# Kernel optimization log

Hardware: AMD Instinct MI355X
Metric: run time of the kernel (lower is better)

Reference implementation:

```python
import jax, jax.numpy as jnp
import numpy as np

N_EMBD = 1024
N_HEAD = 16
HEAD_DIM = N_EMBD // N_HEAD  # 64
LATENT_DIM = N_EMBD // 2     # 512
B, T = 4, 2048


def setup_inputs() -> dict:
    key = jax.random.key(0)
    ks = jax.random.split(key, 5)
    # weights stored [in, out] so forward is x @ W (equivalent to torch Linear with W.T)
    def init(k, fan_in, fan_out):
        bound = 1.0 / np.sqrt(fan_in)
        return jax.random.uniform(k, (fan_in, fan_out), jnp.float32, -bound, bound)
    return {
        "x": jax.random.normal(ks[0], (B, T, N_EMBD), jnp.float32),
        "Wc_down": init(ks[1], N_EMBD, LATENT_DIM),
        "Wq_up": init(ks[2], LATENT_DIM, N_EMBD),
        "Wkv_up": init(ks[3], LATENT_DIM, 2 * HEAD_DIM),
        "Wc_proj": init(ks[4], N_EMBD, N_EMBD),
    }


def reference(x, Wc_down, Wq_up, Wkv_up, Wc_proj):
    Bsz, Tlen, C = x.shape
    latent = x @ Wc_down                                    # [B,T,latent]
    q = (latent @ Wq_up).reshape(Bsz, Tlen, N_HEAD, HEAD_DIM)  # [B,T,H,D]
    kv = latent @ Wkv_up                                    # [B,T,2D]
    k, v = kv[..., :HEAD_DIM], kv[..., HEAD_DIM:]           # shared across heads (MQA)
    scale = 1.0 / np.sqrt(HEAD_DIM)
    att = jnp.einsum("bthd,bsd->bhts", q, k) * scale        # [B,H,T,T]
    causal = jnp.tril(jnp.ones((Tlen, Tlen), dtype=bool))
    att = jnp.where(causal[None, None], att, -jnp.inf)
    att = jax.nn.softmax(att, axis=-1)
    y = jnp.einsum("bhts,bsd->bthd", att, v).reshape(Bsz, Tlen, C)
    return y @ Wc_proj
```

## Files before the change

kernel.cpp:

```cpp
#include <hip/hip_runtime.h>
#include <hip/hip_bf16.h>


typedef __attribute__((ext_vector_type(8))) short bf16x8;
typedef __attribute__((ext_vector_type(4))) float floatx4;

#define B_   4
#define T_   2048
#define C_   1024
#define H_   16
#define D_   64
#define L_   512
#define QKV_N 1152

__device__ __forceinline__ float EXP2F(float x) {
    float r;
    asm("v_exp_f32 %0, %1" : "=v"(r) : "v"(x));
    return r;
}

__device__ __forceinline__ unsigned short f2bf(float f) {
    unsigned int x = __float_as_uint(f);
    unsigned int r = (x + 0x7fffu + ((x >> 16) & 1u)) >> 16;
    return (unsigned short)r;
}

__device__ __forceinline__ unsigned int cvtpk_bf(float lo, float hi) {
    unsigned int r;
    asm("v_cvt_pk_bf16_f32 %0, %1, %2" : "=v"(r) : "v"(lo), "v"(hi));
    return r;
}

__device__ __forceinline__ void gload_lds16(const unsigned short* g, char* l) {
    __builtin_amdgcn_global_load_lds(
        (const __attribute__((address_space(1))) void*)g,
        (__attribute__((address_space(3))) void*)l,
        16, 0, 0);
}

__global__ void cvt_bf16(const float* __restrict__ X, unsigned short* __restrict__ Xb, int n4) {
    int i = blockIdx.x * 256 + threadIdx.x;
    if (i >= n4) return;
    float4 v = *(const float4*)(X + (size_t)i * 4);
    ushort4 o;
    o.x = f2bf(v.x); o.y = f2bf(v.y); o.z = f2bf(v.z); o.w = f2bf(v.w);
    *(ushort4*)(Xb + (size_t)i * 4) = o;
}

__global__ void wtrans(const float* __restrict__ W, unsigned short* __restrict__ Wt,
                       int K, int N, float scale) {
    int idx = blockIdx.x * 256 + threadIdx.x;
    if (idx >= K * N) return;
    int n = idx / K, k = idx - n * K;
    Wt[idx] = f2bf(W[(size_t)k * N + n] * scale);
}

__global__ void vtrans(const unsigned short* __restrict__ qkv, unsigned short* __restrict__ Vt) {
    int idx = blockIdx.x * 256 + threadIdx.x;
    int t = idx & (T_ - 1);
    int d = (idx >> 11) & 63;
    int b = idx >> 17;
    Vt[idx] = qkv[((size_t)(b * T_ + t)) * QKV_N + 1024 + 64 + d];
}

#define BM 128
#define BN 128
#define BK 64

template <bool F32OUT>
__global__ __launch_bounds__(256) void gemm_bt(const unsigned short* __restrict__ A,
                                               const unsigned short* __restrict__ Bt,
                                               void* __restrict__ Cout,
                                               int M, int N, int K) {
    __shared__ __align__(16) char ldsA[BM * BK * 2];
    __shared__ __align__(16) char ldsB[BN * BK * 2];
    const int tid = threadIdx.x;
    const int lane = tid & 63, wave = tid >> 6;
    const int lrow = lane & 15, lhi = lane >> 4;
    const int bm = blockIdx.y * BM, bn = blockIdx.x * BN;
    const int wm = (wave >> 1) * 64, wn = (wave & 1) * 64;

    floatx4 acc[4][4] = {};

    for (int k0 = 0; k0 < K; k0 += BK) {
#pragma unroll
        for (int i = 0; i < 4; ++i) {
            int c = tid + i * 256;
            int row = c >> 3;
            int sc = ((c & 7) ^ (row & 7)) * 8;
            gload_lds16(A + (size_t)(bm + row) * K + k0 + sc,
                        ldsA + (i * 256 + wave * 64) * 16);
            gload_lds16(Bt + (size_t)(bn + row) * K + k0 + sc,
                        ldsB + (i * 256 + wave * 64) * 16);
        }
        __syncthreads();
#pragma unroll
        for (int kk = 0; kk < 2; ++kk) {
            bf16x8 af[4], bfr[4];
#pragma unroll
            for (int m = 0; m < 4; ++m) {
                int row = wm + m * 16 + lrow;
                int colb = kk * 64 + lhi * 16;
                af[m] = *(const bf16x8*)(ldsA + row * 128 + (colb ^ ((row & 7) << 4)));
            }
#pragma unroll
            for (int n = 0; n < 4; ++n) {
                int row = wn + n * 16 + lrow;
                int colb = kk * 64 + lhi * 16;
                bfr[n] = *(const bf16x8*)(ldsB + row * 128 + (colb ^ ((row & 7) << 4)));
            }
#pragma unroll
            for (int m = 0; m < 4; ++m)
#pragma unroll
                for (int n = 0; n < 4; ++n)
                    acc[m][n] = __builtin_amdgcn_mfma_f32_16x16x32_bf16(af[m], bfr[n], acc[m][n], 0, 0, 0);
        }
        __syncthreads();
    }
#pragma unroll
    for (int m = 0; m < 4; ++m)
#pragma unroll
        for (int n = 0; n < 4; ++n)
#pragma unroll
            for (int r = 0; r < 4; ++r) {
                int row = bm + wm + m * 16 + lhi * 4 + r;
                int col = bn + wn + n * 16 + lrow;
                float v = acc[m][n][r];
                if (F32OUT)
                    ((float*)Cout)[(size_t)row * N + col] = v;
                else
                    ((unsigned short*)Cout)[(size_t)row * N + col] = f2bf(v);
            }
}

__global__ __launch_bounds__(256, 2) void flash(const unsigned short* __restrict__ QKV,
                                                const unsigned short* __restrict__ Vt,
                                                unsigned short* __restrict__ Y) {
    const int id = blockIdx.x;
    const int qt = 7 - (id >> 6);
    const int h = (id >> 2) & 15;
    const int b = id & 3;
    const int tid = threadIdx.x;
    const int lane = tid & 63, wave = tid >> 6;
    const int lrow = lane & 15, lhi = lane >> 4;

    __shared__ __align__(16) char ldsK[3][64 * 128];
    __shared__ __align__(16) char ldsV[3][64 * 128];
    __shared__ __align__(16) char ldsP[4][64 * 128];

    const int qbase = qt * 256 + wave * 64;
    const unsigned short* KV = QKV + 1024;
    const int nst = qt * 4 + 4;

    const unsigned short* kp[2];
    const unsigned short* vp[2];
#pragma unroll
    for (int i = 0; i < 2; ++i) {
        int c = tid + i * 256;
        int row = c >> 3;
        int sc = ((c & 7) ^ (row & 7)) * 8;
        kp[i] = KV + ((size_t)(b * T_ + row)) * QKV_N + sc;
        vp[i] = Vt + ((size_t)(b * 64 + row)) * T_ + sc;
    }

    bf16x8 qf[4][2];
#pragma unroll
    for (int nf = 0; nf < 4; ++nf)
#pragma unroll
        for (int kk = 0; kk < 2; ++kk) {
            int trow = b * T_ + qbase + nf * 16 + lrow;
            int col = h * 64 + kk * 32 + lhi * 8;
            qf[nf][kk] = *(const bf16x8*)(QKV + (size_t)trow * QKV_N + col);
        }

    floatx4 o[4][4] = {};
    floatx4 ol[4] = {};

    const short one_bf = (short)0x3F80;
    const bf16x8 ones8 = {one_bf, one_bf, one_bf, one_bf, one_bf, one_bf, one_bf, one_bf};

    char* kcur = ldsK[0];  char* kstg = ldsK[1];  char* kfre = ldsK[2];
    char* vcur = ldsV[0];  char* vstg = ldsV[1];  char* vfre = ldsV[2];
#pragma unroll
    for (int i = 0; i < 2; ++i) {
        gload_lds16(kp[i], kcur + (i * 256 + wave * 64) * 16);
        gload_lds16(vp[i], vcur + (i * 256 + wave * 64) * 16);
        kp[i] += 64 * QKV_N;
        vp[i] += 64;
    }

    for (int st = 0; st < nst; ++st) {
        const bool more = (st + 1 < nst);
        const long kadj = more ? 0 : -(long)(64 * QKV_N);
        const long vadj = more ? 0 : -64L;
#pragma unroll
        for (int i = 0; i < 2; ++i) {
            gload_lds16(kp[i] + kadj, kstg + (i * 256 + wave * 64) * 16);
            gload_lds16(vp[i] + vadj, vstg + (i * 256 + wave * 64) * 16);
        }
        if (more) {
            kp[0] += 64 * QKV_N; kp[1] += 64 * QKV_N;
            vp[0] += 64;         vp[1] += 64;
        }
        asm volatile("s_waitcnt vmcnt(4)" ::: "memory");
        __builtin_amdgcn_s_barrier();
        __builtin_amdgcn_sched_barrier(0);

        if (st * 64 <= qbase + 63) {
            floatx4 s[4][4] = {};
#pragma unroll
            for (int kk = 0; kk < 2; ++kk) {
                bf16x8 kf[4];
#pragma unroll
                for (int mf = 0; mf < 4; ++mf) {
                    int row = mf * 16 + lrow;
                    int colb = kk * 64 + lhi * 16;
                    kf[mf] = *(const bf16x8*)(kcur + row * 128 + (colb ^ ((row & 7) << 4)));
                }
                __builtin_amdgcn_s_setprio(1);
#pragma unroll
                for (int mf = 0; mf < 4; ++mf)
#pragma unroll
                    for (int nf = 0; nf < 4; ++nf)
                        s[mf][nf] = __builtin_amdgcn_mfma_f32_16x16x32_bf16(kf[mf], qf[nf][kk], s[mf][nf], 0, 0, 0);
                __builtin_amdgcn_s_setprio(0);
            }

#pragma unroll
            for (int nf = 0; nf < 4; ++nf) {
                if (st * 64 + 63 > qbase + nf * 16) {
                    int qg = qbase + nf * 16 + lrow;
#pragma unroll
                    for (int mf = 0; mf < 4; ++mf)
#pragma unroll
                        for (int r = 0; r < 4; ++r) {
                            int sg = st * 64 + mf * 16 + lhi * 4 + r;
                            if (sg > qg) s[mf][nf][r] = -1e30f;
                        }
                }
#pragma unroll
                for (int mf = 0; mf < 4; ++mf)
#pragma unroll
                    for (int rr = 0; rr < 4; ++rr)
                        s[mf][nf][rr] = EXP2F(s[mf][nf][rr]);
            }

#pragma unroll
            for (int mf = 0; mf < 4; ++mf)
#pragma unroll
                for (int nf = 0; nf < 4; ++nf) {
                    uint2 pk;
                    pk.x = cvtpk_bf(s[mf][nf][0], s[mf][nf][1]);
                    pk.y = cvtpk_bf(s[mf][nf][2], s[mf][nf][3]);
                    int row = nf * 16 + lrow;
                    int colb = (mf * 16 + lhi * 4) * 2;
                    *(uint2*)(ldsP[wave] + row * 128 + (colb ^ ((row & 7) << 4))) = pk;
                }

#pragma unroll
            for (int ss = 0; ss < 2; ++ss) {
                bf16x8 pf[4], vf[4];
#pragma unroll
                for (int m = 0; m < 4; ++m) {
                    int row = m * 16 + lrow;
                    int colb = ss * 64 + lhi * 16;
                    pf[m] = *(const bf16x8*)(ldsP[wave] + row * 128 + (colb ^ ((row & 7) << 4)));
                }
#pragma unroll
                for (int dn = 0; dn < 4; ++dn) {
                    int row = dn * 16 + lrow;
                    int colb = ss * 64 + lhi * 16;
                    vf[dn] = *(const bf16x8*)(vcur + row * 128 + (colb ^ ((row & 7) << 4)));
                }
                __builtin_amdgcn_s_setprio(1);
#pragma unroll
                for (int m = 0; m < 4; ++m) {
#pragma unroll
                    for (int dn = 0; dn < 4; ++dn)
                        o[m][dn] = __builtin_amdgcn_mfma_f32_16x16x32_bf16(pf[m], vf[dn], o[m][dn], 0, 0, 0);
                    ol[m] = __builtin_amdgcn_mfma_f32_16x16x32_bf16(pf[m], ones8, ol[m], 0, 0, 0);
                }
                __builtin_amdgcn_s_setprio(0);
            }
        }

        char* t;
        t = kcur; kcur = kstg; kstg = kfre; kfre = t;
        t = vcur; vcur = vstg; vstg = vfre; vfre = t;
    }

#pragma unroll
    for (int m = 0; m < 4; ++m) {
        float linv[4];
#pragma unroll
        for (int rr = 0; rr < 4; ++rr) linv[rr] = __builtin_amdgcn_rcpf(ol[m][rr]);
#pragma unroll
        for (int dn = 0; dn < 4; ++dn)
#pragma unroll
            for (int rr = 0; rr < 4; ++rr) {
                int trow = b * T_ + qbase + m * 16 + lhi * 4 + rr;
                int col = h * 64 + dn * 16 + lrow;
                Y[(size_t)trow * C_ + col] = f2bf(o[m][dn][rr] * linv[rr]);
            }
    }
}

extern "C" void kernel_launch(void* const* d_in, const int* in_sizes, int n_in,
                              void* d_out, int out_size, void* d_ws, size_t ws_size,
                              hipStream_t stream) {
    (void)in_sizes; (void)n_in; (void)out_size; (void)ws_size;
    const float* x   = (const float*)d_in[0];
    const float* Wd  = (const float*)d_in[1];
    const float* Wq  = (const float*)d_in[2];
    const float* Wkv = (const float*)d_in[3];
    const float* Wp  = (const float*)d_in[4];
    float* out = (float*)d_out;
    char* ws = (char*)d_ws;

    const int BT = B_ * T_;
    const float KSC = 0.125f * 1.44269504f;

    unsigned short* xb     = (unsigned short*)(ws + 0);
    unsigned short* wdT    = (unsigned short*)(ws + 16777216);
    unsigned short* wqkvT  = (unsigned short*)(ws + 17825792);
    unsigned short* wpT    = (unsigned short*)(ws + 19005440);
    unsigned short* latent = (unsigned short*)(ws + 21102592);
    unsigned short* qkv    = (unsigned short*)(ws + 29491200);
    unsigned short* vt     = (unsigned short*)(ws + 48365568);
    unsigned short* yb     = xb;

    cvt_bf16<<<(BT * C_ / 4 + 255) / 256, 256, 0, stream>>>(x, xb, BT * C_ / 4);
    wtrans<<<(C_ * L_ + 255) / 256, 256, 0, stream>>>(Wd, wdT, C_, L_, 1.0f);
    wtrans<<<(L_ * C_ + 255) / 256, 256, 0, stream>>>(Wq, wqkvT, L_, C_, KSC);
    wtrans<<<(L_ * 128 + 255) / 256, 256, 0, stream>>>(Wkv, wqkvT + 1024 * 512, L_, 128, 1.0f);
    wtrans<<<(C_ * C_ + 255) / 256, 256, 0, stream>>>(Wp, wpT, C_, C_, 1.0f);

    gemm_bt<false><<<dim3(L_ / BN, BT / BM), 256, 0, stream>>>(xb, wdT, latent, BT, L_, C_);
    gemm_bt<false><<<dim3(QKV_N / BN, BT / BM), 256, 0, stream>>>(latent, wqkvT, qkv, BT, QKV_N, L_);

    vtrans<<<(B_ * 64 * T_ + 255) / 256, 256, 0, stream>>>(qkv, vt);

    flash<<<512, 256, 0, stream>>>(qkv, vt, yb);

    gemm_bt<true><<<dim3(C_ / BN, BT / BM), 256, 0, stream>>>(yb, wpT, out, BT, C_, C_);
}
```

Measured before the change: 156.5 us.

## Double-buffer GEMM LDS, shrink flash query tiles, pass P via permlane swaps

The GEMM now double-buffers its A/B LDS tiles and prefetches the next K slice while computing the current one, so load latency overlaps with MFMA work. The flash kernel halves the query tile per block (128 rows, 32 per wave) and doubles the grid to 1024 blocks with occupancy 3, aiming for better load balance across the causal triangle. The P matrix is rearranged in registers with permlane32/16 swaps instead of a round trip through LDS, which removes the ldsP buffer and its writes and reads. In exchange, smaller query tiles mean each K/V tile is loaded more times, and the GEMM uses twice the LDS.

```diff
diff --git a/kernel.cpp b/kernel.cpp
--- a/kernel.cpp
+++ b/kernel.cpp
@@ -4,6 +4,7 @@
 
 typedef __attribute__((ext_vector_type(8))) short bf16x8;
 typedef __attribute__((ext_vector_type(4))) float floatx4;
+typedef __attribute__((ext_vector_type(4))) unsigned int uintx4;
 
 #define B_   4
 #define T_   2048
@@ -31,6 +32,13 @@
     return r;
 }
 
+__device__ __forceinline__ void pl32(unsigned int& d, unsigned int& s) {
+    asm("v_permlane32_swap_b32 %0, %1" : "+v"(d), "+v"(s));
+}
+__device__ __forceinline__ void pl16(unsigned int& d, unsigned int& s) {
+    asm("v_permlane16_swap_b32 %0, %1" : "+v"(d), "+v"(s));
+}
+
 __device__ __forceinline__ void gload_lds16(const unsigned short* g, char* l) {
     __builtin_amdgcn_global_load_lds(
         (const __attribute__((address_space(1))) void*)g,
@@ -72,28 +80,50 @@
                                                const unsigned short* __restrict__ Bt,
                                                void* __restrict__ Cout,
                                                int M, int N, int K) {
-    __shared__ __align__(16) char ldsA[BM * BK * 2];
-    __shared__ __align__(16) char ldsB[BN * BK * 2];
+    __shared__ __align__(16) char ldsA[2][BM * BK * 2];
+    __shared__ __align__(16) char ldsB[2][BN * BK * 2];
     const int tid = threadIdx.x;
     const int lane = tid & 63, wave = tid >> 6;
     const int lrow = lane & 15, lhi = lane >> 4;
     const int bm = blockIdx.y * BM, bn = blockIdx.x * BN;
     const int wm = (wave >> 1) * 64, wn = (wave & 1) * 64;
 
+    const unsigned short* ap[4];
+    const unsigned short* bp[4];
+#pragma unroll
+    for (int i = 0; i < 4; ++i) {
+        int c = tid + i * 256;
+        int row = c >> 3;
+        int sc = ((c & 7) ^ (row & 7)) * 8;
+        ap[i] = A + (size_t)(bm + row) * K + sc;
+        bp[i] = Bt + (size_t)(bn + row) * K + sc;
+    }
+    const int nk = K >> 6;
     floatx4 acc[4][4] = {};
 
-    for (int k0 = 0; k0 < K; k0 += BK) {
-#pragma unroll
-        for (int i = 0; i < 4; ++i) {
-            int c = tid + i * 256;
-            int row = c >> 3;
-            int sc = ((c & 7) ^ (row & 7)) * 8;
-            gload_lds16(A + (size_t)(bm + row) * K + k0 + sc,
-                        ldsA + (i * 256 + wave * 64) * 16);
-            gload_lds16(Bt + (size_t)(bn + row) * K + k0 + sc,
-                        ldsB + (i * 256 + wave * 64) * 16);
-        }
-        __syncthreads();
+#pragma unroll
+    for (int i = 0; i < 4; ++i) {
+        gload_lds16(ap[i], ldsA[0] + (i * 256 + wave * 64) * 16);
+        gload_lds16(bp[i], ldsB[0] + (i * 256 + wave * 64) * 16);
+        ap[i] += BK; bp[i] += BK;
+    }
+
+    for (int t = 0; t < nk; ++t) {
+        const int cur = t & 1;
+        if (t + 1 < nk) {
+#pragma unroll
+            for (int i = 0; i < 4; ++i) {
+                gload_lds16(ap[i], ldsA[cur ^ 1] + (i * 256 + wave * 64) * 16);
+                gload_lds16(bp[i], ldsB[cur ^ 1] + (i * 256 + wave * 64) * 16);
+                ap[i] += BK; bp[i] += BK;
+            }
+            asm volatile("s_waitcnt vmcnt(8)" ::: "memory");
+        } else {
+            asm volatile("s_waitcnt vmcnt(0)" ::: "memory");
+        }
+        __builtin_amdgcn_s_barrier();
+        __builtin_amdgcn_sched_barrier(0);
+
 #pragma unroll
         for (int kk = 0; kk < 2; ++kk) {
             bf16x8 af[4], bfr[4];
@@ -101,13 +131,13 @@
             for (int m = 0; m < 4; ++m) {
                 int row = wm + m * 16 + lrow;
                 int colb = kk * 64 + lhi * 16;
-                af[m] = *(const bf16x8*)(ldsA + row * 128 + (colb ^ ((row & 7) << 4)));
+                af[m] = *(const bf16x8*)(ldsA[cur] + row * 128 + (colb ^ ((row & 7) << 4)));
             }
 #pragma unroll
             for (int n = 0; n < 4; ++n) {
                 int row = wn + n * 16 + lrow;
                 int colb = kk * 64 + lhi * 16;
-                bfr[n] = *(const bf16x8*)(ldsB + row * 128 + (colb ^ ((row & 7) << 4)));
+                bfr[n] = *(const bf16x8*)(ldsB[cur] + row * 128 + (colb ^ ((row & 7) << 4)));
             }
 #pragma unroll
             for (int m = 0; m < 4; ++m)
@@ -115,7 +145,8 @@
                 for (int n = 0; n < 4; ++n)
                     acc[m][n] = __builtin_amdgcn_mfma_f32_16x16x32_bf16(af[m], bfr[n], acc[m][n], 0, 0, 0);
         }
-        __syncthreads();
+        __builtin_amdgcn_sched_barrier(0);
+        __builtin_amdgcn_s_barrier();
     }
 #pragma unroll
     for (int m = 0; m < 4; ++m)
@@ -133,11 +164,11 @@
             }
 }
 
-__global__ __launch_bounds__(256, 2) void flash(const unsigned short* __restrict__ QKV,
+__global__ __launch_bounds__(256, 3) void flash(const unsigned short* __restrict__ QKV,
                                                 const unsigned short* __restrict__ Vt,
                                                 unsigned short* __restrict__ Y) {
     const int id = blockIdx.x;
-    const int qt = 7 - (id >> 6);
+    const int qt = 15 - (id >> 6);
     const int h = (id >> 2) & 15;
     const int b = id & 3;
     const int tid = threadIdx.x;
@@ -146,11 +177,10 @@
 
     __shared__ __align__(16) char ldsK[3][64 * 128];
     __shared__ __align__(16) char ldsV[3][64 * 128];
-    __shared__ __align__(16) char ldsP[4][64 * 128];
-
-    const int qbase = qt * 256 + wave * 64;
+
+    const int qbase = qt * 128 + wave * 32;
     const unsigned short* KV = QKV + 1024;
-    const int nst = qt * 4 + 4;
+    const int nst = qt * 2 + 2;
 
     const unsigned short* kp[2];
     const unsigned short* vp[2];
@@ -163,9 +193,9 @@
         vp[i] = Vt + ((size_t)(b * 64 + row)) * T_ + sc;
     }
 
-    bf16x8 qf[4][2];
-#pragma unroll
-    for (int nf = 0; nf < 4; ++nf)
+    bf16x8 qf[2][2];
+#pragma unroll
+    for (int nf = 0; nf < 2; ++nf)
 #pragma unroll
         for (int kk = 0; kk < 2; ++kk) {
             int trow = b * T_ + qbase + nf * 16 + lrow;
@@ -173,8 +203,8 @@
             qf[nf][kk] = *(const bf16x8*)(QKV + (size_t)trow * QKV_N + col);
         }
 
-    floatx4 o[4][4] = {};
-    floatx4 ol[4] = {};
+    floatx4 o[2][4] = {};
+    floatx4 ol[2] = {};
 
     const short one_bf = (short)0x3F80;
     const bf16x8 ones8 = {one_bf, one_bf, one_bf, one_bf, one_bf, one_bf, one_bf, one_bf};
@@ -206,8 +236,8 @@
         __builtin_amdgcn_s_barrier();
         __builtin_amdgcn_sched_barrier(0);
 
-        if (st * 64 <= qbase + 63) {
-            floatx4 s[4][4] = {};
+        if (st * 64 <= qbase + 31) {
+            floatx4 s[4][2] = {};
 #pragma unroll
             for (int kk = 0; kk < 2; ++kk) {
                 bf16x8 kf[4];
@@ -221,13 +251,13 @@
 #pragma unroll
                 for (int mf = 0; mf < 4; ++mf)
 #pragma unroll
-                    for (int nf = 0; nf < 4; ++nf)
+                    for (int nf = 0; nf < 2; ++nf)
                         s[mf][nf] = __builtin_amdgcn_mfma_f32_16x16x32_bf16(kf[mf], qf[nf][kk], s[mf][nf], 0, 0, 0);
                 __builtin_amdgcn_s_setprio(0);
             }
 
 #pragma unroll
-            for (int nf = 0; nf < 4; ++nf) {
+            for (int nf = 0; nf < 2; ++nf) {
                 if (st * 64 + 63 > qbase + nf * 16) {
                     int qg = qbase + nf * 16 + lrow;
 #pragma unroll
@@ -245,27 +275,24 @@
                         s[mf][nf][rr] = EXP2F(s[mf][nf][rr]);
             }
 
-#pragma unroll
-            for (int mf = 0; mf < 4; ++mf)
-#pragma unroll
-                for (int nf = 0; nf < 4; ++nf) {
-                    uint2 pk;
-                    pk.x = cvtpk_bf(s[mf][nf][0], s[mf][nf][1]);
-                    pk.y = cvtpk_bf(s[mf][nf][2], s[mf][nf][3]);
-                    int row = nf * 16 + lrow;
-                    int colb = (mf * 16 + lhi * 4) * 2;
-                    *(uint2*)(ldsP[wave] + row * 128 + (colb ^ ((row & 7) << 4))) = pk;
+            bf16x8 pfr[2][2];
+#pragma unroll
+            for (int nf = 0; nf < 2; ++nf)
+#pragma unroll
+                for (int ss = 0; ss < 2; ++ss) {
+                    unsigned int A0 = cvtpk_bf(s[2 * ss][nf][0], s[2 * ss][nf][1]);
+                    unsigned int A1 = cvtpk_bf(s[2 * ss][nf][2], s[2 * ss][nf][3]);
+                    unsigned int B0 = cvtpk_bf(s[2 * ss + 1][nf][0], s[2 * ss + 1][nf][1]);
+                    unsigned int B1 = cvtpk_bf(s[2 * ss + 1][nf][2], s[2 * ss + 1][nf][3]);
+                    pl32(A0, B0); pl16(A0, B0);
+                    pl32(A1, B1); pl16(A1, B1);
+                    uintx4 pw; pw.x = A0; pw.y = A1; pw.z = B0; pw.w = B1;
+                    pfr[nf][ss] = __builtin_bit_cast(bf16x8, pw);
                 }
 
 #pragma unroll
             for (int ss = 0; ss < 2; ++ss) {
-                bf16x8 pf[4], vf[4];
-#pragma unroll
-                for (int m = 0; m < 4; ++m) {
-                    int row = m * 16 + lrow;
-                    int colb = ss * 64 + lhi * 16;
-                    pf[m] = *(const bf16x8*)(ldsP[wave] + row * 128 + (colb ^ ((row & 7) << 4)));
-                }
+                bf16x8 vf[4];
 #pragma unroll
                 for (int dn = 0; dn < 4; ++dn) {
                     int row = dn * 16 + lrow;
@@ -274,11 +301,11 @@
                 }
                 __builtin_amdgcn_s_setprio(1);
 #pragma unroll
-                for (int m = 0; m < 4; ++m) {
+                for (int m = 0; m < 2; ++m) {
 #pragma unroll
                     for (int dn = 0; dn < 4; ++dn)
-                        o[m][dn] = __builtin_amdgcn_mfma_f32_16x16x32_bf16(pf[m], vf[dn], o[m][dn], 0, 0, 0);
-                    ol[m] = __builtin_amdgcn_mfma_f32_16x16x32_bf16(pf[m], ones8, ol[m], 0, 0, 0);
+                        o[m][dn] = __builtin_amdgcn_mfma_f32_16x16x32_bf16(pfr[m][ss], vf[dn], o[m][dn], 0, 0, 0);
+                    ol[m] = __builtin_amdgcn_mfma_f32_16x16x32_bf16(pfr[m][ss], ones8, ol[m], 0, 0, 0);
                 }
                 __builtin_amdgcn_s_setprio(0);
             }
@@ -290,7 +317,7 @@
     }
 
 #pragma unroll
-    for (int m = 0; m < 4; ++m) {
+    for (int m = 0; m < 2; ++m) {
         float linv[4];
 #pragma unroll
         for (int rr = 0; rr < 4; ++rr) linv[rr] = __builtin_amdgcn_rcpf(ol[m][rr]);
@@ -340,7 +367,7 @@
 
     vtrans<<<(B_ * 64 * T_ + 255) / 256, 256, 0, stream>>>(qkv, vt);
 
-    flash<<<512, 256, 0, stream>>>(qkv, vt, yb);
+    flash<<<1024, 256, 0, stream>>>(qkv, vt, yb);
 
     gemm_bt<true><<<dim3(C_ / BN, BT / BM), 256, 0, stream>>>(yb, wpT, out, BT, C_, C_);
 }
```

Result: faster. 145.4 us (-7.1%).
